# Optimization experiments

Measured on AMD Instinct MI355X. Metric: run time of the kernel, lower is better.

Reference implementation:

```python
import jax, jax.numpy as jnp
import numpy as np

B, C, N = 4, 256, 4096
DQK = C // 8

def setup_inputs() -> dict:
    key = jax.random.key(0)
    ks = jax.random.split(key, 8)
    s = 1.0 / np.sqrt(C)
    x = jax.random.normal(ks[0], (B, C, N), dtype=jnp.float32)
    Wq = jax.random.normal(ks[1], (DQK, C), dtype=jnp.float32) * s
    bq = jax.random.normal(ks[2], (DQK,), dtype=jnp.float32) * s
    Wk = jax.random.normal(ks[3], (DQK, C), dtype=jnp.float32) * s
    bk = jax.random.normal(ks[4], (DQK,), dtype=jnp.float32) * s
    Wv = jax.random.normal(ks[5], (C, C), dtype=jnp.float32) * s
    bv = jax.random.normal(ks[6], (C,), dtype=jnp.float32) * s
    gamma = jnp.ones((1,), dtype=jnp.float32) * 0.5  # nonzero so residual path is exercised
    return {"x": x, "Wq": Wq, "bq": bq, "Wk": Wk, "bk": bk, "Wv": Wv, "bv": bv, "gamma": gamma}

def reference(x, Wq, bq, Wk, bk, Wv, bv, gamma):
    # 1x1 conv == channel matmul: [d, C] @ [B, C, N] -> [B, d, N]
    q = jnp.einsum('dc,bcn->bdn', Wq, x) + bq[None, :, None]
    k = jnp.einsum('dc,bcn->bdn', Wk, x) + bk[None, :, None]
    v = jnp.einsum('oc,bcn->bon', Wv, x) + bv[None, :, None]
    # energy[b,i,j] = sum_d q[b,d,i] * k[b,d,j]  -> [B, N, N]
    energy = jnp.einsum('bdi,bdj->bij', q, k)
    attention = jax.nn.softmax(energy, axis=-1)
    # out = bmm(v, attention^T): out[b,c,i] = sum_j v[b,c,j] * attention[b,i,j]
    out = jnp.einsum('bcj,bij->bci', v, attention)
    out = gamma[0] * out + x
    return (out, attention)
```

## Files before the change

### kernel.cpp

```cpp
#include <hip/hip_runtime.h>

#define NB 4
#define NCH 256
#define NTOK 4096

typedef _Float16 f16x4 __attribute__((ext_vector_type(4)));
typedef _Float16 f16x8 __attribute__((ext_vector_type(8)));
typedef __fp16 h16x2 __attribute__((ext_vector_type(2)));
typedef float f32x4 __attribute__((ext_vector_type(4)));

union F2H  { h16x2 h; int i; };
union U64  { uint2 u; f16x4 h; int2 i2; };

#define LDS_BARRIER() asm volatile("s_waitcnt lgkmcnt(0)\n\ts_barrier" ::: "memory")

__global__ __launch_bounds__(256) void wpack_kernel(
    const float* __restrict__ Wq, const float* __restrict__ Wk,
    const float* __restrict__ Wv, _Float16* __restrict__ W16)
{
    int g = blockIdx.x * 256 + threadIdx.x;
    if (g >= 320 * 64) return;
    int o = g >> 6, c4 = g & 63;
    const float* src = (o < 32) ? (Wq + o * NCH) :
                       (o < 64) ? (Wk + (o - 32) * NCH) : (Wv + (o - 64) * NCH);
    float4 v = ((const float4*)src)[c4];
    f16x4 p;
    p[0] = (_Float16)v.x; p[1] = (_Float16)v.y;
    p[2] = (_Float16)v.z; p[3] = (_Float16)v.w;
    *(f16x4*)(W16 + (size_t)o * NCH + c4 * 4) = p;
}

__global__ __launch_bounds__(256) void qkv_mfma_kernel(
    const float* __restrict__ x, const _Float16* __restrict__ W16,
    const float* __restrict__ bq, const float* __restrict__ bk,
    const float* __restrict__ bv,
    _Float16* __restrict__ qkT, _Float16* __restrict__ vbuf)
{
    __shared__ char xs[32 * 512];
    __shared__ _Float16 vls[256 * 36];
    const int tid = threadIdx.x;
    const int b = blockIdx.x & 3;
    const int n0 = (blockIdx.x >> 2) << 5;
    const float* xb = x + (size_t)b * NCH * NTOK + n0;

    {
        const int c4 = tid & 63, no = tid >> 6;
        float vals[4][8];
        #pragma unroll
        for (int u = 0; u < 4; ++u) {
            const float* xr = xb + (size_t)(c4 * 4 + u) * NTOK + no * 8;
            float4 a = *(const float4*)xr;
            float4 b2 = *(const float4*)(xr + 4);
            vals[u][0]=a.x; vals[u][1]=a.y; vals[u][2]=a.z; vals[u][3]=a.w;
            vals[u][4]=b2.x; vals[u][5]=b2.y; vals[u][6]=b2.z; vals[u][7]=b2.w;
        }
        #pragma unroll
        for (int j = 0; j < 8; ++j) {
            const int n = no * 8 + j;
            f16x4 pk;
            pk[0]=(_Float16)vals[0][j]; pk[1]=(_Float16)vals[1][j];
            pk[2]=(_Float16)vals[2][j]; pk[3]=(_Float16)vals[3][j];
            *(f16x4*)(xs + n * 512 + ((c4 * 8) ^ ((n & 7) << 4))) = pk;
        }
    }
    __syncthreads();

    const int w = tid >> 6, l = tid & 63;
    const int iofs = l & 15, h = l >> 4;

    f32x4 acc[5][2];
    #pragma unroll
    for (int ot = 0; ot < 5; ++ot)
        #pragma unroll
        for (int nt = 0; nt < 2; ++nt) acc[ot][nt] = (f32x4){0.f,0.f,0.f,0.f};

    #pragma unroll
    for (int kk = 0; kk < 8; ++kk) {
        f16x8 bf[2];
        #pragma unroll
        for (int nt = 0; nt < 2; ++nt) {
            const int n = nt * 16 + iofs;
            bf[nt] = *(const f16x8*)(xs + n * 512 + ((kk * 64 + h * 16) ^ ((n & 7) << 4)));
        }
        #pragma unroll
        for (int ot = 0; ot < 5; ++ot) {
            const int og = w * 5 + ot;
            f16x8 af = *(const f16x8*)(W16 + (size_t)(og * 16 + iofs) * NCH + kk * 32 + h * 8);
            #pragma unroll
            for (int nt = 0; nt < 2; ++nt)
                acc[ot][nt] = __builtin_amdgcn_mfma_f32_16x16x32_f16(af, bf[nt], acc[ot][nt], 0, 0, 0);
        }
    }

    #pragma unroll
    for (int ot = 0; ot < 5; ++ot) {
        const int og = w * 5 + ot;
        float4 bias;
        if (og < 2)      bias = *(const float4*)(bq + og * 16 + 4 * h);
        else if (og < 4) bias = *(const float4*)(bk + (og - 2) * 16 + 4 * h);
        else             bias = *(const float4*)(bv + (og - 4) * 16 + 4 * h);
        #pragma unroll
        for (int nt = 0; nt < 2; ++nt) {
            const int n = n0 + nt * 16 + iofs;
            f32x4 a = acc[ot][nt];
            if (og < 4) {
                f16x4 pk;
                pk[0] = (_Float16)(a[0] + bias.x); pk[1] = (_Float16)(a[1] + bias.y);
                pk[2] = (_Float16)(a[2] + bias.z); pk[3] = (_Float16)(a[3] + bias.w);
                const int col = (og < 2) ? (og * 16 + 4 * h) : (32 + (og - 2) * 16 + 4 * h);
                *(f16x4*)(qkT + (size_t)(b * NTOK + n) * 64 + col) = pk;
            } else {
                const int vr0 = (og - 4) * 16 + 4 * h;
                const int nl = nt * 16 + iofs;
                const float bb[4] = {bias.x, bias.y, bias.z, bias.w};
                #pragma unroll
                for (int r = 0; r < 4; ++r)
                    vls[(vr0 + r) * 36 + nl] = (_Float16)(a[r] + bb[r]);
            }
        }
    }
    __syncthreads();
    {
        const int vr = tid >> 2;
        const int piece = tid & 3;
        #pragma unroll
        for (int pass = 0; pass < 4; ++pass) {
            const int row = pass * 64 + vr;
            f16x8 val = *(const f16x8*)(&vls[row * 36 + piece * 8]);
            *(f16x8*)(vbuf + (size_t)(b * NCH + row) * NTOK + n0 + piece * 8) = val;
        }
    }
}

__global__ __launch_bounds__(256) void rowsum_kernel(
    const _Float16* __restrict__ qkT, float* __restrict__ rs_sum)
{
    const int bid = blockIdx.x;
    const int b = bid >> 9;
    const int rem = bid & 511;
    const int ib = rem >> 3, js = rem & 7;
    const int tid = threadIdx.x;
    const int w = tid >> 6, l = tid & 63;
    const int iofs = l & 15, h = l >> 4;
    const int i16 = ib * 64 + w * 16;
    const int j0 = js * 512;
    const _Float16* qk_b = qkT + (size_t)b * NTOK * 64;

    f16x8 qfrag = *(const f16x8*)(qk_b + (size_t)(i16 + iofs) * 64 + h * 8);
    float sums[4] = {0.f, 0.f, 0.f, 0.f};
    const f32x4 zero = {0.f, 0.f, 0.f, 0.f};
    #pragma unroll 4
    for (int jt = 0; jt < 32; ++jt) {
        f16x8 kfrag = *(const f16x8*)(qk_b + (size_t)(j0 + jt*16 + iofs) * 64 + 32 + h * 8);
        f32x4 s = __builtin_amdgcn_mfma_f32_16x16x32_f16(kfrag, qfrag, zero, 0, 0, 0);
        #pragma unroll
        for (int r = 0; r < 4; ++r) sums[r] += __expf(s[r]);
    }
    float tot = sums[0] + sums[1] + sums[2] + sums[3];
    tot += __shfl_xor(tot, 16, 64);
    tot += __shfl_xor(tot, 32, 64);
    if (l < 16) atomicAdd(&rs_sum[b * NTOK + i16 + iofs], tot);
}

__global__ __launch_bounds__(1024, 1) void attn_pv_kernel(
    const _Float16* __restrict__ qkT, const _Float16* __restrict__ vbuf,
    const float* __restrict__ rs_sum, const float* __restrict__ x,
    const float* __restrict__ gamma, float* __restrict__ out, float* __restrict__ atn)
{
    __shared__ char P[2][64 * 512];
    const int tid = threadIdx.x;
    const int w = tid >> 6, l = tid & 63;
    const int iofs = l & 15, h = l >> 4;
    const int xk = blockIdx.x & 7, rest = blockIdx.x >> 3;
    const int b = xk >> 1;
    const int itb = (rest << 1) | (xk & 1);
    const int i0 = itb << 6;

    const _Float16* qk_b = qkT + (size_t)b * NTOK * 64;
    const _Float16* v_b  = vbuf + (size_t)b * NCH * NTOK;
    float* atn_b = atn + (size_t)b * NTOK * NTOK;
    const int c0w = w * 16;
    const float LOG2E = 1.44269504f;

    f16x8 qfrag[4];
    float rsl[4];
    #pragma unroll
    for (int ig = 0; ig < 4; ++ig) {
        qfrag[ig] = *(const f16x8*)(qk_b + (size_t)(i0 + ig*16 + iofs) * 64 + h * 8);
        rsl[ig] = -__log2f(rs_sum[b * NTOK + i0 + ig*16 + iofs]);
    }

    const f32x4 zero = {0.f, 0.f, 0.f, 0.f};
    f32x4 acc[4];
    #pragma unroll
    for (int ig = 0; ig < 4; ++ig) acc[ig] = zero;

    auto phaseA = [&](int chunk, int buf) {
        const int jg = chunk * 256 + w * 16;
        f16x8 kfrag = *(const f16x8*)(qk_b + (size_t)(jg + iofs) * 64 + 32 + h * 8);
        #pragma unroll
        for (int ig = 0; ig < 4; ++ig) {
            f32x4 s = __builtin_amdgcn_mfma_f32_16x16x32_f16(kfrag, qfrag[ig], zero, 0, 0, 0);
            f32x4 pv;
            #pragma unroll
            for (int r = 0; r < 4; ++r)
                pv[r] = __builtin_amdgcn_exp2f(__builtin_fmaf(s[r], LOG2E, rsl[ig]));
            F2H p0, p1;
            p0.h = __builtin_amdgcn_cvt_pkrtz(pv[0], pv[1]);
            p1.h = __builtin_amdgcn_cvt_pkrtz(pv[2], pv[3]);
            const int iloc = ig * 16 + iofs;
            const int jloc = w * 16 + 4 * h;
            const int byte = iloc * 512 + ((jloc * 2) ^ ((iloc & 7) << 4));
            U64 u; u.i2.x = p0.i; u.i2.y = p1.i;
            *(int2*)(P[buf] + byte) = u.i2;
        }
    };

    auto phaseW = [&](int chunk, int buf) {
        const int lane16 = tid & 15;
        const int row = tid >> 4;
        const int sw = (row & 7) << 4;
        float* arow = atn_b + (size_t)(i0 + row) * NTOK + chunk * 256;
        #pragma unroll
        for (int u = 0; u < 4; ++u) {
            const int jf = u * 64 + lane16 * 4;
            U64 v; v.i2 = *(const int2*)(P[buf] + row * 512 + ((jf * 2) ^ sw));
            f32x4 st = {(float)v.h[0], (float)v.h[1], (float)v.h[2], (float)v.h[3]};
            __builtin_nontemporal_store(st, (f32x4*)(arow + jf));
        }
    };

    auto phaseB = [&](int chunk, int buf) {
        const int cj0 = chunk * 256;
        #pragma unroll 4
        for (int ks = 0; ks < 8; ++ks) {
            f16x8 pfrag[4];
            #pragma unroll
            for (int ig = 0; ig < 4; ++ig) {
                const int iloc = ig * 16 + iofs;
                const int byte = iloc * 512 + ((ks * 64 + h * 16) ^ ((iloc & 7) << 4));
                pfrag[ig] = *(const f16x8*)(P[buf] + byte);
            }
            const int jg = cj0 + ks * 32 + h * 8;
            f16x8 vfrag = *(const f16x8*)(v_b + (size_t)(c0w + iofs) * NTOK + jg);
            #pragma unroll
            for (int ig = 0; ig < 4; ++ig)
                acc[ig] = __builtin_amdgcn_mfma_f32_16x16x32_f16(vfrag, pfrag[ig], acc[ig], 0, 0, 0);
        }
    };

    phaseA(0, 0);
    LDS_BARRIER();
    for (int c = 0; c < 16; ++c) {
        if (c < 15) phaseA(c + 1, (c + 1) & 1);
        phaseB(c, c & 1);
        __builtin_amdgcn_sched_barrier(0);
        phaseW(c, c & 1);
        LDS_BARRIER();
    }

    const float g2 = gamma[0];
    #pragma unroll
    for (int ig = 0; ig < 4; ++ig) {
        #pragma unroll
        for (int r = 0; r < 4; ++r) {
            const int c = c0w + 4*h + r;
            const size_t bse = ((size_t)(b * NCH + c)) * NTOK + i0 + ig*16 + iofs;
            out[bse] = g2 * acc[ig][r] + x[bse];
        }
    }
}

extern "C" void kernel_launch(void* const* d_in, const int* in_sizes, int n_in,
                              void* d_out, int out_size, void* d_ws, size_t ws_size,
                              hipStream_t stream) {
    const float* x     = (const float*)d_in[0];
    const float* Wq    = (const float*)d_in[1];
    const float* bq    = (const float*)d_in[2];
    const float* Wk    = (const float*)d_in[3];
    const float* bk    = (const float*)d_in[4];
    const float* Wv    = (const float*)d_in[5];
    const float* bv    = (const float*)d_in[6];
    const float* gamma = (const float*)d_in[7];

    float* out = (float*)d_out;
    float* atn = out + (size_t)NB * NCH * NTOK;

    _Float16* qkT  = (_Float16*)d_ws;
    _Float16* vbuf = qkT + (size_t)NB * NTOK * 64;
    float* rs_sum  = (float*)(vbuf + (size_t)NB * NCH * NTOK);
    _Float16* W16  = (_Float16*)(rs_sum + NB * NTOK);

    hipMemsetAsync(rs_sum, 0, (size_t)NB * NTOK * sizeof(float), stream);
    wpack_kernel<<<80, 256, 0, stream>>>(Wq, Wk, Wv, W16);
    qkv_mfma_kernel<<<512, 256, 0, stream>>>(x, W16, bq, bk, bv, qkT, vbuf);
    rowsum_kernel<<<2048, 256, 0, stream>>>(qkT, rs_sum);
    attn_pv_kernel<<<256, 1024, 0, stream>>>(qkT, vbuf, rs_sum, x, gamma, out, atn);
}
```

Baseline: 152.0 us.

## Enlarge attention row tile to 128 and split channels and K across waves

Each block of the P·V kernel now handles 128 query rows and one half of the 256 output channels. Its 16 waves are arranged as 8 channel slices times 2 K-halves, and the two K-halves are combined through LDS at the end. Attention-matrix writes alternate between the two channel-half blocks by chunk, so each row tile's probabilities are stored only once. The aim is more reuse of V fragments per loaded P tile and less redundant work per block. The cost is double the LDS, more registers (8 accumulators plus 8 q fragments), and duplicated QK/exp work across the two channel-half blocks.

```diff
diff --git a/kernel.cpp b/kernel.cpp
--- a/kernel.cpp
+++ b/kernel.cpp
@@ -167,44 +167,49 @@
     const float* __restrict__ rs_sum, const float* __restrict__ x,
     const float* __restrict__ gamma, float* __restrict__ out, float* __restrict__ atn)
 {
-    __shared__ char P[2][64 * 512];
+    __shared__ char P[2][128 * 512];
     const int tid = threadIdx.x;
     const int w = tid >> 6, l = tid & 63;
     const int iofs = l & 15, h = l >> 4;
-    const int xk = blockIdx.x & 7, rest = blockIdx.x >> 3;
-    const int b = xk >> 1;
-    const int itb = (rest << 1) | (xk & 1);
-    const int i0 = itb << 6;
+    const int id = blockIdx.x;
+    const int xk = id & 7;
+    const int b  = xk >> 1;
+    const int rest = id >> 3;
+    const int ch = rest & 1;
+    const int itb = ((rest >> 1) << 1) | (xk & 1);
+    const int i0 = itb << 7;
 
     const _Float16* qk_b = qkT + (size_t)b * NTOK * 64;
     const _Float16* v_b  = vbuf + (size_t)b * NCH * NTOK;
     float* atn_b = atn + (size_t)b * NTOK * NTOK;
-    const int c0w = w * 16;
+    const int s = w >> 1;
+    const int khalf = w & 1;
+    const int c0w = ch * 128 + s * 16;
     const float LOG2E = 1.44269504f;
 
-    f16x8 qfrag[4];
-    float rsl[4];
-    #pragma unroll
-    for (int ig = 0; ig < 4; ++ig) {
+    f16x8 qfrag[8];
+    float rsl[8];
+    #pragma unroll
+    for (int ig = 0; ig < 8; ++ig) {
         qfrag[ig] = *(const f16x8*)(qk_b + (size_t)(i0 + ig*16 + iofs) * 64 + h * 8);
         rsl[ig] = -__log2f(rs_sum[b * NTOK + i0 + ig*16 + iofs]);
     }
 
     const f32x4 zero = {0.f, 0.f, 0.f, 0.f};
-    f32x4 acc[4];
-    #pragma unroll
-    for (int ig = 0; ig < 4; ++ig) acc[ig] = zero;
+    f32x4 acc[8];
+    #pragma unroll
+    for (int ig = 0; ig < 8; ++ig) acc[ig] = zero;
 
     auto phaseA = [&](int chunk, int buf) {
         const int jg = chunk * 256 + w * 16;
         f16x8 kfrag = *(const f16x8*)(qk_b + (size_t)(jg + iofs) * 64 + 32 + h * 8);
         #pragma unroll
-        for (int ig = 0; ig < 4; ++ig) {
-            f32x4 s = __builtin_amdgcn_mfma_f32_16x16x32_f16(kfrag, qfrag[ig], zero, 0, 0, 0);
+        for (int ig = 0; ig < 8; ++ig) {
+            f32x4 sv = __builtin_amdgcn_mfma_f32_16x16x32_f16(kfrag, qfrag[ig], zero, 0, 0, 0);
             f32x4 pv;
             #pragma unroll
             for (int r = 0; r < 4; ++r)
-                pv[r] = __builtin_amdgcn_exp2f(__builtin_fmaf(s[r], LOG2E, rsl[ig]));
+                pv[r] = __builtin_amdgcn_exp2f(__builtin_fmaf(sv[r], LOG2E, rsl[ig]));
             F2H p0, p1;
             p0.h = __builtin_amdgcn_cvt_pkrtz(pv[0], pv[1]);
             p1.h = __builtin_amdgcn_cvt_pkrtz(pv[2], pv[3]);
@@ -217,14 +222,15 @@
     };
 
     auto phaseW = [&](int chunk, int buf) {
-        const int lane16 = tid & 15;
-        const int row = tid >> 4;
+        const int lg = tid & 7;
+        const int row = tid >> 3;
         const int sw = (row & 7) << 4;
         float* arow = atn_b + (size_t)(i0 + row) * NTOK + chunk * 256;
-        #pragma unroll
-        for (int u = 0; u < 4; ++u) {
-            const int jf = u * 64 + lane16 * 4;
-            U64 v; v.i2 = *(const int2*)(P[buf] + row * 512 + ((jf * 2) ^ sw));
+        const char* prow = P[buf] + row * 512;
+        #pragma unroll
+        for (int u = 0; u < 8; ++u) {
+            const int jf = u * 32 + lg * 4;
+            U64 v; v.i2 = *(const int2*)(prow + ((jf * 2) ^ sw));
             f32x4 st = {(float)v.h[0], (float)v.h[1], (float)v.h[2], (float)v.h[3]};
             __builtin_nontemporal_store(st, (f32x4*)(arow + jf));
         }
@@ -232,20 +238,18 @@
 
     auto phaseB = [&](int chunk, int buf) {
         const int cj0 = chunk * 256;
-        #pragma unroll 4
-        for (int ks = 0; ks < 8; ++ks) {
-            f16x8 pfrag[4];
-            #pragma unroll
-            for (int ig = 0; ig < 4; ++ig) {
+        #pragma unroll
+        for (int kk = 0; kk < 4; ++kk) {
+            const int ks = khalf * 4 + kk;
+            const int jg = cj0 + ks * 32 + h * 8;
+            f16x8 vfrag = *(const f16x8*)(v_b + (size_t)(c0w + iofs) * NTOK + jg);
+            #pragma unroll
+            for (int ig = 0; ig < 8; ++ig) {
                 const int iloc = ig * 16 + iofs;
                 const int byte = iloc * 512 + ((ks * 64 + h * 16) ^ ((iloc & 7) << 4));
-                pfrag[ig] = *(const f16x8*)(P[buf] + byte);
+                f16x8 pfrag = *(const f16x8*)(P[buf] + byte);
+                acc[ig] = __builtin_amdgcn_mfma_f32_16x16x32_f16(vfrag, pfrag, acc[ig], 0, 0, 0);
             }
-            const int jg = cj0 + ks * 32 + h * 8;
-            f16x8 vfrag = *(const f16x8*)(v_b + (size_t)(c0w + iofs) * NTOK + jg);
-            #pragma unroll
-            for (int ig = 0; ig < 4; ++ig)
-                acc[ig] = __builtin_amdgcn_mfma_f32_16x16x32_f16(vfrag, pfrag[ig], acc[ig], 0, 0, 0);
         }
     };
 
@@ -255,18 +259,32 @@
         if (c < 15) phaseA(c + 1, (c + 1) & 1);
         phaseB(c, c & 1);
         __builtin_amdgcn_sched_barrier(0);
-        phaseW(c, c & 1);
+        if (ch == (c & 1)) phaseW(c, c & 1);
         LDS_BARRIER();
     }
 
-    const float g2 = gamma[0];
-    #pragma unroll
-    for (int ig = 0; ig < 4; ++ig) {
-        #pragma unroll
-        for (int r = 0; r < 4; ++r) {
-            const int c = c0w + 4*h + r;
-            const size_t bse = ((size_t)(b * NCH + c)) * NTOK + i0 + ig*16 + iofs;
-            out[bse] = g2 * acc[ig][r] + x[bse];
+    {
+        float* red = (float*)P[0];
+        if (khalf) {
+            #pragma unroll
+            for (int ig = 0; ig < 8; ++ig)
+                #pragma unroll
+                for (int r = 0; r < 4; ++r)
+                    red[s * 2048 + (ig * 4 + r) * 64 + l] = acc[ig][r];
+        }
+        LDS_BARRIER();
+        if (!khalf) {
+            const float g2 = gamma[0];
+            #pragma unroll
+            for (int ig = 0; ig < 8; ++ig) {
+                #pragma unroll
+                for (int r = 0; r < 4; ++r) {
+                    float a2 = acc[ig][r] + red[s * 2048 + (ig * 4 + r) * 64 + l];
+                    const int c = c0w + 4*h + r;
+                    const size_t bse = ((size_t)(b * NCH + c)) * NTOK + i0 + ig*16 + iofs;
+                    out[bse] = g2 * a2 + x[bse];
+                }
+            }
         }
     }
 }
```

Result: faster. 145.4 us, median of 2 (-4.4%).
